# Kernel optimization log

Hardware: AMD Instinct MI355X
Metric: run time of the kernel (lower is better)

The kernel has to match this reference:

```python
import jax, jax.numpy as jnp
import numpy as np

N_USERS = 50000
N_ITEMS = 100000
N = N_USERS + N_ITEMS
E = 4_800_000
D = 64
N_LAYERS = 3
LEAKY = 0.5  # HGCNConv is built with leaky=0.5
LN_EPS = 1e-5


def setup_inputs() -> dict:
    key = jax.random.key(0)
    k1, k2, k3, k4 = jax.random.split(key, 4)
    ego = jax.random.normal(k1, (N, D), dtype=jnp.float32)
    vals = jax.random.uniform(k2, (E,), dtype=jnp.float32)
    rows = jax.random.randint(k3, (E,), 0, N, dtype=jnp.int32)
    cols = jax.random.randint(k4, (E,), 0, N, dtype=jnp.int32)
    gamma = jnp.ones((D,), dtype=jnp.float32)
    beta = jnp.zeros((D,), dtype=jnp.float32)
    return {"ego": ego, "vals": vals, "gamma": gamma, "beta": beta,
            "rows": rows, "cols": cols}


def _spmm(rows, cols, vals, x):
    # y[r] += vals[e] * x[cols[e]]  -> sparse NxN adj @ x ([N, D])
    return jax.ops.segment_sum(vals[:, None] * x[cols], rows, num_segments=N)


def _spmm_t(rows, cols, vals, x):
    # adj.T @ x : roles of rows/cols swapped
    return jax.ops.segment_sum(vals[:, None] * x[rows], cols, num_segments=N)


def _two_hop(rows, cols, vals, x):
    # sparse.mm(adj, sparse.mm(adj.t(), x))
    return _spmm(rows, cols, vals, _spmm_t(rows, cols, vals, x))


def _layer_norm(x, gamma, beta):
    mu = jnp.mean(x, axis=-1, keepdims=True)
    var = jnp.mean(jnp.square(x - mu), axis=-1, keepdims=True)
    return (x - mu) * jax.lax.rsqrt(var + LN_EPS) * gamma + beta


def reference(ego, vals, gamma, beta, rows, cols):
    res = ego
    e = ego
    for k in range(N_LAYERS):
        if k != N_LAYERS - 1:
            # HGCNConv with LeakyReLU(0.5)
            e = jax.nn.leaky_relu(_two_hop(rows, cols, vals, e), negative_slope=LEAKY)
        else:
            # final layer: LN(conv(adj, e, act=False)) + residual
            e = _layer_norm(_two_hop(rows, cols, vals, e), gamma, beta) + res
    # final embeddings [N, D]; user part = e[:N_USERS], item part = e[N_USERS:]
    return e
```

## Files before the change

### kernel.cpp

```cpp
#include <hip/hip_runtime.h>
#include <hip/hip_fp16.h>


#define NTOT 150000
#define NE   4800000
#define DD   64
#define NB   147
#define NBLK 512
#define EPB  9375

__global__ __launch_bounds__(256) void k_hist(const int* __restrict__ rows,
                                              const int* __restrict__ cols,
                                              int* __restrict__ histR,
                                              int* __restrict__ histC) {
    __shared__ int hR[NB], hC[NB];
    const int tid = threadIdx.x, blk = blockIdx.x;
    for (int i = tid; i < NB; i += 256) { hR[i] = 0; hC[i] = 0; }
    __syncthreads();
    const int e0 = blk * EPB;
    const int e1 = min(NE, e0 + EPB);
    for (int e = e0 + tid; e < e1; e += 256) {
        atomicAdd(&hR[rows[e] >> 10], 1);
        atomicAdd(&hC[cols[e] >> 10], 1);
    }
    __syncthreads();
    for (int i = tid; i < NB; i += 256) {
        histR[i * NBLK + blk] = hR[i];
        histC[i * NBLK + blk] = hC[i];
    }
}

__global__ __launch_bounds__(1024) void k_scan2(int* __restrict__ hR, int* __restrict__ hC,
                                                int* __restrict__ bbR, int* __restrict__ bbC) {
    __shared__ int wtot[16], wexcl[16];
    __shared__ int ctot;
    int* a  = blockIdx.x ? hC  : hR;
    int* bb = blockIdx.x ? bbC : bbR;
    const int n = NB * NBLK;
    const int tid  = threadIdx.x;
    const int lane = tid & 63, wv = tid >> 6;
    int carry = 0;
    for (int base = 0; base < n; base += 1024) {
        const int i = base + tid;
        const int v = (i < n) ? a[i] : 0;
        int s = v;
        #pragma unroll
        for (int off = 1; off < 64; off <<= 1) {
            int t = __shfl_up(s, off);
            if (lane >= off) s += t;
        }
        if (lane == 63) wtot[wv] = s;
        __syncthreads();
        if (tid == 0) {
            int run = 0;
            #pragma unroll
            for (int w = 0; w < 16; ++w) { wexcl[w] = run; run += wtot[w]; }
            ctot = run;
        }
        __syncthreads();
        if (i < n) a[i] = carry + wexcl[wv] + (s - v);
        carry += ctot;
        __syncthreads();
    }
    for (int i = tid; i <= NB; i += 1024) bb[i] = (i < NB) ? a[i * NBLK] : NE;
}

__global__ __launch_bounds__(256) void k_bin(const int* __restrict__ rows,
                                             const int* __restrict__ cols,
                                             const float* __restrict__ vals,
                                             const int* __restrict__ histR,
                                             const int* __restrict__ histC,
                                             int2* __restrict__ binR,
                                             int2* __restrict__ binC) {
    __shared__ int cR[NB], cC[NB];
    const int tid = threadIdx.x, blk = blockIdx.x;
    for (int i = tid; i < NB; i += 256) {
        cR[i] = histR[i * NBLK + blk];
        cC[i] = histC[i * NBLK + blk];
    }
    __syncthreads();
    const int e0 = blk * EPB;
    const int e1 = min(NE, e0 + EPB);
    for (int e = e0 + tid; e < e1; e += 256) {
        const int r = rows[e], c = cols[e];
        const int vb = __float_as_int(vals[e]);
        int p = atomicAdd(&cR[r >> 10], 1);
        int2 pr; pr.x = ((r & 1023) << 18) | c; pr.y = vb;
        binR[p] = pr;
        int q = atomicAdd(&cC[c >> 10], 1);
        int2 pc; pc.x = ((c & 1023) << 18) | r; pc.y = vb;
        binC[q] = pc;
    }
}

__global__ __launch_bounds__(1024) void k_sort(const int* __restrict__ bbR,
                                               const int2* __restrict__ binR,
                                               int2* __restrict__ csr, int* __restrict__ startsR,
                                               const int* __restrict__ bbC,
                                               const int2* __restrict__ binC,
                                               int2* __restrict__ csc, int* __restrict__ startsC) {
    __shared__ int hist[1024];
    __shared__ int cur[1024];
    __shared__ int wtot[16], wexcl[16];
    const int tid = threadIdx.x;
    const int lane = tid & 63, wv = tid >> 6;
    const int dir = (blockIdx.x >= NB) ? 1 : 0;
    const int b = blockIdx.x - dir * NB;
    const int*  bb     = dir ? bbC     : bbR;
    const int2* bin    = dir ? binC    : binR;
    int2*       out    = dir ? csc     : csr;
    int*        starts = dir ? startsC : startsR;
    const int ebase = bb[b];
    const int eend  = bb[b + 1];
    hist[tid] = 0;
    __syncthreads();
    for (int i = ebase + tid; i < eend; i += 1024)
        atomicAdd(&hist[((unsigned)bin[i].x) >> 18], 1);
    __syncthreads();
    const int v = hist[tid];
    int s = v;
    #pragma unroll
    for (int off = 1; off < 64; off <<= 1) { int t = __shfl_up(s, off); if (lane >= off) s += t; }
    if (lane == 63) wtot[wv] = s;
    __syncthreads();
    if (tid == 0) { int run = 0; for (int w = 0; w < 16; ++w) { wexcl[w] = run; run += wtot[w]; } }
    __syncthreads();
    const int excl = ebase + wexcl[wv] + (s - v);
    const int r0 = b << 10;
    if (r0 + tid < NTOT) starts[r0 + tid] = excl;
    cur[tid] = excl;
    __syncthreads();
    for (int i = ebase + tid; i < eend; i += 1024) {
        const int2 ed = bin[i];
        const int lr = ((unsigned)ed.x) >> 18;
        const int pos = atomicAdd(&cur[lr], 1);
        int2 o; o.x = ed.x & 0x3FFFF; o.y = ed.y;
        out[pos] = o;
    }
    if (blockIdx.x == 0 && tid == 0) { startsR[NTOT] = NE; startsC[NTOT] = NE; }
}

__global__ __launch_bounds__(256) void k_cvt(const float2* __restrict__ x,
                                             __half2* __restrict__ y, int n2) {
    int i = blockIdx.x * 256 + threadIdx.x;
    if (i < n2) y[i] = __float22half2_rn(x[i]);
}

template <int MODE>
__global__ __launch_bounds__(256) void k_spmm_h(const int* __restrict__ starts,
                                                const int2* __restrict__ edges,
                                                const __half2* __restrict__ xh,
                                                __half2* __restrict__ yh,
                                                float* __restrict__ yf,
                                                const float* __restrict__ gamma,
                                                const float* __restrict__ beta,
                                                const float* __restrict__ ego) {
    const int gid  = blockIdx.x * 256 + threadIdx.x;
    const int wid  = gid >> 6;
    const int lane = threadIdx.x & 63;
    if (wid >= NTOT) return;
    const int half_id = lane >> 5;
    const int c2 = lane & 31;
    const int s  = starts[wid];
    const int e2 = starts[wid + 1];
    float ax = 0.f, ay = 0.f;
    for (int base = s; base < e2; base += 64) {
        const int idx = base + lane;
        int2 ed;
        if (idx < e2) ed = edges[idx]; else { ed.x = 0; ed.y = 0; }
        int nb = e2 - base; if (nb > 64) nb = 64;
        const int npair = (nb + 1) >> 1;
        #pragma unroll 4
        for (int j = 0; j < npair; ++j) {
            const int sel = 2 * j + half_id;
            const int   c = __shfl(ed.x, sel);
            const float v = __int_as_float(__shfl(ed.y, sel));
            const float2 f = __half22float2(xh[c * 32 + c2]);
            ax = fmaf(v, f.x, ax);
            ay = fmaf(v, f.y, ay);
        }
    }
    ax += __shfl_xor(ax, 32);
    ay += __shfl_xor(ay, 32);
    if (MODE == 0) {
        if (lane < 32) yh[wid * 32 + c2] = __floats2half2_rn(ax, ay);
    } else if (MODE == 1) {
        if (lane < 32) {
            const float bx = ax > 0.f ? ax : 0.5f * ax;
            const float by = ay > 0.f ? ay : 0.5f * ay;
            yh[wid * 32 + c2] = __floats2half2_rn(bx, by);
        }
    } else {
        float s1 = ax + ay;
        #pragma unroll
        for (int off = 32; off; off >>= 1) s1 += __shfl_xor(s1, off);
        const float mu = s1 * (1.f / 128.f);
        const float dx = ax - mu, dy = ay - mu;
        float q = dx * dx + dy * dy;
        #pragma unroll
        for (int off = 32; off; off >>= 1) q += __shfl_xor(q, off);
        const float rs = rsqrtf(q * (1.f / 128.f) + 1e-5f);
        if (lane < 32) {
            const float2 g2 = ((const float2*)gamma)[c2];
            const float2 b2 = ((const float2*)beta)[c2];
            const float2 eg = ((const float2*)ego)[wid * 32 + c2];
            float2 o;
            o.x = dx * rs * g2.x + b2.x + eg.x;
            o.y = dy * rs * g2.y + b2.y + eg.y;
            ((float2*)yf)[wid * 32 + c2] = o;
        }
    }
}

__global__ __launch_bounds__(256) void k_push(const int* __restrict__ src_idx,
                                              const int* __restrict__ dst_idx,
                                              const float* __restrict__ vals,
                                              const float* __restrict__ x,
                                              float* __restrict__ y) {
    int gid  = blockIdx.x * 256 + threadIdx.x;
    int e    = gid >> 6;
    int lane = gid & 63;
    if (e >= NE) return;
    atomicAdd(&y[dst_idx[e] * DD + lane], vals[e] * x[src_idx[e] * DD + lane]);
}

__global__ __launch_bounds__(256) void k_leaky(float* __restrict__ x, int n) {
    int i = blockIdx.x * 256 + threadIdx.x;
    if (i < n) { float v = x[i]; x[i] = v > 0.f ? v : 0.5f * v; }
}

__global__ __launch_bounds__(256) void k_ln(const float* __restrict__ z,
                                            const float* __restrict__ gamma,
                                            const float* __restrict__ beta,
                                            const float* __restrict__ ego,
                                            float* __restrict__ out) {
    int gid  = blockIdx.x * 256 + threadIdx.x;
    int wid  = gid >> 6;
    int lane = threadIdx.x & 63;
    if (wid >= NTOT) return;
    float v = z[wid * DD + lane];
    float sum = v;
    #pragma unroll
    for (int off = 32; off; off >>= 1) sum += __shfl_xor(sum, off);
    float mu = sum * (1.f / 64.f);
    float d  = v - mu;
    float vs = d * d;
    #pragma unroll
    for (int off = 32; off; off >>= 1) vs += __shfl_xor(vs, off);
    float rs = rsqrtf(vs * (1.f / 64.f) + 1e-5f);
    out[wid * DD + lane] = d * rs * gamma[lane] + beta[lane] + ego[wid * DD + lane];
}

extern "C" void kernel_launch(void* const* d_in, const int* in_sizes, int n_in,
                              void* d_out, int out_size, void* d_ws, size_t ws_size,
                              hipStream_t stream) {
    const float* ego   = (const float*)d_in[0];
    const float* vals  = (const float*)d_in[1];
    const float* gamma = (const float*)d_in[2];
    const float* beta  = (const float*)d_in[3];
    const int*   rows  = (const int*)d_in[4];
    const int*   cols  = (const int*)d_in[5];
    float* out = (float*)d_out;

    const size_t SEG   = (size_t)NE * 8;
    const size_t SMETA = 600064;
    const size_t NEED  = 3 * SEG + 2 * SMETA + 1280;

    if (ws_size >= NEED) {
        char* w = (char*)d_ws;
        int2* csr  = (int2*)w;
        int2* csc  = (int2*)(w + SEG);
        int2* binR = (int2*)(w + 2 * SEG);
        int2* binC = (int2*)d_out;
        int* histR = (int*)w;
        int* histC = (int*)(w + SEG);
        int* startsR = (int*)(w + 3 * SEG);
        int* startsC = (int*)(w + 3 * SEG + SMETA);
        int* bbR     = (int*)(w + 3 * SEG + 2 * SMETA);
        int* bbC     = bbR + (NB + 1);
        __half2* B1h  = (__half2*)(w + 2 * SEG);
        __half2* B2h  = (__half2*)(w + 2 * SEG + SEG / 2);
        __half2* egoh = (__half2*)d_out;

        k_hist <<<NBLK, 256, 0, stream>>>(rows, cols, histR, histC);
        k_scan2<<<2, 1024, 0, stream>>>(histR, histC, bbR, bbC);
        k_bin  <<<NBLK, 256, 0, stream>>>(rows, cols, vals, histR, histC, binR, binC);
        k_sort <<<2 * NB, 1024, 0, stream>>>(bbR, binR, csr, startsR, bbC, binC, csc, startsC);
        k_cvt  <<<(NTOT * DD / 2 + 255) / 256, 256, 0, stream>>>((const float2*)ego, egoh, NTOT * DD / 2);

        const int GRID_N = (NTOT * 64) / 256;
        k_spmm_h<0><<<GRID_N, 256, 0, stream>>>(startsC, csc, egoh, B1h, nullptr, nullptr, nullptr, nullptr);
        k_spmm_h<1><<<GRID_N, 256, 0, stream>>>(startsR, csr, B1h, B2h, nullptr, nullptr, nullptr, nullptr);
        k_spmm_h<0><<<GRID_N, 256, 0, stream>>>(startsC, csc, B2h, B1h, nullptr, nullptr, nullptr, nullptr);
        k_spmm_h<1><<<GRID_N, 256, 0, stream>>>(startsR, csr, B1h, B2h, nullptr, nullptr, nullptr, nullptr);
        k_spmm_h<0><<<GRID_N, 256, 0, stream>>>(startsC, csc, B2h, B1h, nullptr, nullptr, nullptr, nullptr);
        k_spmm_h<2><<<GRID_N, 256, 0, stream>>>(startsR, csr, B1h, nullptr, out, gamma, beta, ego);
    } else {
        const size_t FEAT_BYTES = (size_t)NTOT * DD * 4;
        float* B1 = (float*)d_ws;
        float* B2 = out;
        const int GRID_P = NE / 4;
        const int GRID_N = (NTOT * DD) / 256;
        const float* e = ego;
        for (int layer = 0; layer < 3; ++layer) {
            hipMemsetAsync(B1, 0, FEAT_BYTES, stream);
            k_push<<<GRID_P, 256, 0, stream>>>(rows, cols, vals, e, B1);
            hipMemsetAsync(B2, 0, FEAT_BYTES, stream);
            k_push<<<GRID_P, 256, 0, stream>>>(cols, rows, vals, B1, B2);
            if (layer < 2) {
                k_leaky<<<GRID_N, 256, 0, stream>>>(B2, NTOT * DD);
                e = B2;
            } else {
                k_ln<<<GRID_N, 256, 0, stream>>>(B2, gamma, beta, ego, out);
            }
        }
    }
}
```

Baseline: 1.375 ms.

## Split fp16 features into column halves and gather 16-byte chunks per edge

The fp16 feature matrix is stored as two 32-column halves, each 64 bytes per row, and each SpMM pass now runs once per half. Each lane loads an int4 holding 8 halves, so 16 edges are processed at once per wavefront instead of 2. The intent is a smaller gathered working set per pass for better cache hit rates, plus wider loads that keep more gathers in flight. In exchange, the edge lists are read twice per layer, more kernels are launched, and more cross-lane shuffle reductions are needed. The final layer-norm kernel reads both halves and also uses 8-wide edge groups.

```diff
diff --git a/kernel.cpp b/kernel.cpp
--- a/kernel.cpp
+++ b/kernel.cpp
@@ -8,6 +8,8 @@
 #define NB   147
 #define NBLK 512
 #define EPB  9375
+#define HALF_I4 (NTOT * 4)
+#define HALF_H2 (NTOT * 16)
 
 __global__ __launch_bounds__(256) void k_hist(const int* __restrict__ rows,
                                               const int* __restrict__ cols,
@@ -141,17 +143,72 @@
 }
 
 __global__ __launch_bounds__(256) void k_cvt(const float2* __restrict__ x,
-                                             __half2* __restrict__ y, int n2) {
+                                             __half2* __restrict__ y) {
     int i = blockIdx.x * 256 + threadIdx.x;
-    if (i < n2) y[i] = __float22half2_rn(x[i]);
+    const int r = i >> 5, j = i & 31;
+    const int half = j >> 4;
+    y[half * HALF_H2 + r * 16 + (j & 15)] = __float22half2_rn(x[i]);
 }
 
 template <int MODE>
-__global__ __launch_bounds__(256) void k_spmm_h(const int* __restrict__ starts,
+__global__ __launch_bounds__(256) void k_spmm_s(const int* __restrict__ starts,
                                                 const int2* __restrict__ edges,
-                                                const __half2* __restrict__ xh,
-                                                __half2* __restrict__ yh,
-                                                float* __restrict__ yf,
+                                                const int4* __restrict__ xh,
+                                                int4* __restrict__ yh) {
+    const int gid  = blockIdx.x * 256 + threadIdx.x;
+    const int wid  = gid >> 6;
+    const int lane = threadIdx.x & 63;
+    if (wid >= NTOT) return;
+    const int g = lane >> 2;
+    const int l = lane & 3;
+    const int s  = starts[wid];
+    const int e2 = starts[wid + 1];
+    float acc[8];
+    #pragma unroll
+    for (int k = 0; k < 8; ++k) acc[k] = 0.f;
+    for (int base = s; base < e2; base += 64) {
+        const int idx = base + lane;
+        int2 ed;
+        if (idx < e2) ed = edges[idx]; else { ed.x = 0; ed.y = 0; }
+        const int nb = min(e2 - base, 64);
+        for (int j = 0; j < nb; j += 16) {
+            const int sel = j + g;
+            const int   c = __shfl(ed.x, sel);
+            const float v = __int_as_float(__shfl(ed.y, sel));
+            const int4 q = xh[c * 4 + l];
+            const __half2* h2 = (const __half2*)&q;
+            #pragma unroll
+            for (int k = 0; k < 4; ++k) {
+                const float2 f = __half22float2(h2[k]);
+                acc[2 * k]     = fmaf(v, f.x, acc[2 * k]);
+                acc[2 * k + 1] = fmaf(v, f.y, acc[2 * k + 1]);
+            }
+        }
+    }
+    #pragma unroll
+    for (int off = 4; off < 64; off <<= 1) {
+        #pragma unroll
+        for (int k = 0; k < 8; ++k) acc[k] += __shfl_xor(acc[k], off);
+    }
+    if (l == lane) {
+        __half2 o[4];
+        #pragma unroll
+        for (int k = 0; k < 4; ++k) {
+            float a = acc[2 * k], b = acc[2 * k + 1];
+            if (MODE == 1) {
+                a = a > 0.f ? a : 0.5f * a;
+                b = b > 0.f ? b : 0.5f * b;
+            }
+            o[k] = __floats2half2_rn(a, b);
+        }
+        yh[wid * 4 + l] = *(const int4*)o;
+    }
+}
+
+__global__ __launch_bounds__(256) void k_spmm_f(const int* __restrict__ starts,
+                                                const int2* __restrict__ edges,
+                                                const int4* __restrict__ xh,
+                                                float* __restrict__ out,
                                                 const float* __restrict__ gamma,
                                                 const float* __restrict__ beta,
                                                 const float* __restrict__ ego) {
@@ -159,55 +216,66 @@
     const int wid  = gid >> 6;
     const int lane = threadIdx.x & 63;
     if (wid >= NTOT) return;
-    const int half_id = lane >> 5;
-    const int c2 = lane & 31;
+    const int g = lane >> 3;
+    const int l = lane & 7;
+    const int hoff = (l >> 2) * HALF_I4 + (l & 3);
     const int s  = starts[wid];
     const int e2 = starts[wid + 1];
-    float ax = 0.f, ay = 0.f;
+    float acc[8];
+    #pragma unroll
+    for (int k = 0; k < 8; ++k) acc[k] = 0.f;
     for (int base = s; base < e2; base += 64) {
         const int idx = base + lane;
         int2 ed;
         if (idx < e2) ed = edges[idx]; else { ed.x = 0; ed.y = 0; }
-        int nb = e2 - base; if (nb > 64) nb = 64;
-        const int npair = (nb + 1) >> 1;
-        #pragma unroll 4
-        for (int j = 0; j < npair; ++j) {
-            const int sel = 2 * j + half_id;
+        const int nb = min(e2 - base, 64);
+        for (int j = 0; j < nb; j += 8) {
+            const int sel = j + g;
             const int   c = __shfl(ed.x, sel);
             const float v = __int_as_float(__shfl(ed.y, sel));
-            const float2 f = __half22float2(xh[c * 32 + c2]);
-            ax = fmaf(v, f.x, ax);
-            ay = fmaf(v, f.y, ay);
-        }
-    }
-    ax += __shfl_xor(ax, 32);
-    ay += __shfl_xor(ay, 32);
-    if (MODE == 0) {
-        if (lane < 32) yh[wid * 32 + c2] = __floats2half2_rn(ax, ay);
-    } else if (MODE == 1) {
-        if (lane < 32) {
-            const float bx = ax > 0.f ? ax : 0.5f * ax;
-            const float by = ay > 0.f ? ay : 0.5f * ay;
-            yh[wid * 32 + c2] = __floats2half2_rn(bx, by);
-        }
-    } else {
-        float s1 = ax + ay;
-        #pragma unroll
-        for (int off = 32; off; off >>= 1) s1 += __shfl_xor(s1, off);
-        const float mu = s1 * (1.f / 128.f);
-        const float dx = ax - mu, dy = ay - mu;
-        float q = dx * dx + dy * dy;
-        #pragma unroll
-        for (int off = 32; off; off >>= 1) q += __shfl_xor(q, off);
-        const float rs = rsqrtf(q * (1.f / 128.f) + 1e-5f);
-        if (lane < 32) {
-            const float2 g2 = ((const float2*)gamma)[c2];
-            const float2 b2 = ((const float2*)beta)[c2];
-            const float2 eg = ((const float2*)ego)[wid * 32 + c2];
-            float2 o;
-            o.x = dx * rs * g2.x + b2.x + eg.x;
-            o.y = dy * rs * g2.y + b2.y + eg.y;
-            ((float2*)yf)[wid * 32 + c2] = o;
+            const int4 q = xh[c * 4 + hoff];
+            const __half2* h2 = (const __half2*)&q;
+            #pragma unroll
+            for (int k = 0; k < 4; ++k) {
+                const float2 f = __half22float2(h2[k]);
+                acc[2 * k]     = fmaf(v, f.x, acc[2 * k]);
+                acc[2 * k + 1] = fmaf(v, f.y, acc[2 * k + 1]);
+            }
+        }
+    }
+    #pragma unroll
+    for (int off = 8; off < 64; off <<= 1) {
+        #pragma unroll
+        for (int k = 0; k < 8; ++k) acc[k] += __shfl_xor(acc[k], off);
+    }
+    float s1 = 0.f;
+    #pragma unroll
+    for (int k = 0; k < 8; ++k) s1 += acc[k];
+    #pragma unroll
+    for (int off = 1; off < 8; off <<= 1) s1 += __shfl_xor(s1, off);
+    const float mu = s1 * (1.f / 64.f);
+    float d[8], q2 = 0.f;
+    #pragma unroll
+    for (int k = 0; k < 8; ++k) { d[k] = acc[k] - mu; q2 += d[k] * d[k]; }
+    #pragma unroll
+    for (int off = 1; off < 8; off <<= 1) q2 += __shfl_xor(q2, off);
+    const float rs = rsqrtf(q2 * (1.f / 64.f) + 1e-5f);
+    if (lane < 8) {
+        const float4* g4 = (const float4*)gamma;
+        const float4* b4 = (const float4*)beta;
+        const float4* e4 = (const float4*)ego + (size_t)wid * 16;
+        float4*       o4 = (float4*)out + (size_t)wid * 16;
+        #pragma unroll
+        for (int half = 0; half < 2; ++half) {
+            const float4 gg = g4[2 * l + half];
+            const float4 bb = b4[2 * l + half];
+            const float4 ee = e4[2 * l + half];
+            float4 o;
+            o.x = d[4 * half + 0] * rs * gg.x + bb.x + ee.x;
+            o.y = d[4 * half + 1] * rs * gg.y + bb.y + ee.y;
+            o.z = d[4 * half + 2] * rs * gg.z + bb.z + ee.z;
+            o.w = d[4 * half + 3] * rs * gg.w + bb.w + ee.w;
+            o4[2 * l + half] = o;
         }
     }
 }
@@ -278,23 +346,28 @@
         int* startsC = (int*)(w + 3 * SEG + SMETA);
         int* bbR     = (int*)(w + 3 * SEG + 2 * SMETA);
         int* bbC     = bbR + (NB + 1);
-        __half2* B1h  = (__half2*)(w + 2 * SEG);
-        __half2* B2h  = (__half2*)(w + 2 * SEG + SEG / 2);
-        __half2* egoh = (__half2*)d_out;
+        int4* B1 = (int4*)(w + 2 * SEG);
+        int4* B2 = (int4*)(w + 2 * SEG + SEG / 2);
+        int4* EG = (int4*)d_out;
 
         k_hist <<<NBLK, 256, 0, stream>>>(rows, cols, histR, histC);
         k_scan2<<<2, 1024, 0, stream>>>(histR, histC, bbR, bbC);
         k_bin  <<<NBLK, 256, 0, stream>>>(rows, cols, vals, histR, histC, binR, binC);
         k_sort <<<2 * NB, 1024, 0, stream>>>(bbR, binR, csr, startsR, bbC, binC, csc, startsC);
-        k_cvt  <<<(NTOT * DD / 2 + 255) / 256, 256, 0, stream>>>((const float2*)ego, egoh, NTOT * DD / 2);
+        k_cvt  <<<(NTOT * 32) / 256, 256, 0, stream>>>((const float2*)ego, (__half2*)EG);
 
         const int GRID_N = (NTOT * 64) / 256;
-        k_spmm_h<0><<<GRID_N, 256, 0, stream>>>(startsC, csc, egoh, B1h, nullptr, nullptr, nullptr, nullptr);
-        k_spmm_h<1><<<GRID_N, 256, 0, stream>>>(startsR, csr, B1h, B2h, nullptr, nullptr, nullptr, nullptr);
-        k_spmm_h<0><<<GRID_N, 256, 0, stream>>>(startsC, csc, B2h, B1h, nullptr, nullptr, nullptr, nullptr);
-        k_spmm_h<1><<<GRID_N, 256, 0, stream>>>(startsR, csr, B1h, B2h, nullptr, nullptr, nullptr, nullptr);
-        k_spmm_h<0><<<GRID_N, 256, 0, stream>>>(startsC, csc, B2h, B1h, nullptr, nullptr, nullptr, nullptr);
-        k_spmm_h<2><<<GRID_N, 256, 0, stream>>>(startsR, csr, B1h, nullptr, out, gamma, beta, ego);
+        for (int h = 0; h < 2; ++h)
+            k_spmm_s<0><<<GRID_N, 256, 0, stream>>>(startsC, csc, EG + h * HALF_I4, B1 + h * HALF_I4);
+        for (int h = 0; h < 2; ++h)
+            k_spmm_s<1><<<GRID_N, 256, 0, stream>>>(startsR, csr, B1 + h * HALF_I4, B2 + h * HALF_I4);
+        for (int h = 0; h < 2; ++h)
+            k_spmm_s<0><<<GRID_N, 256, 0, stream>>>(startsC, csc, B2 + h * HALF_I4, B1 + h * HALF_I4);
+        for (int h = 0; h < 2; ++h)
+            k_spmm_s<1><<<GRID_N, 256, 0, stream>>>(startsR, csr, B1 + h * HALF_I4, B2 + h * HALF_I4);
+        for (int h = 0; h < 2; ++h)
+            k_spmm_s<0><<<GRID_N, 256, 0, stream>>>(startsC, csc, B2 + h * HALF_I4, B1 + h * HALF_I4);
+        k_spmm_f<<<GRID_N, 256, 0, stream>>>(startsR, csr, B1, out, gamma, beta, ego);
     } else {
         const size_t FEAT_BYTES = (size_t)NTOT * DD * 4;
         float* B1 = (float*)d_ws;
```

Result: faster. 1.283 ms (-6.6%).

## Compress edges to 32-bit with 14-bit quantized weights and slice features into column chunks

Applied to the files above, without the earlier changes.

Edges are packed into one u32 each: an 18-bit neighbor index plus a 14-bit quantized value, replacing the 8-byte int2, which halves edge traffic. Features are stored scaled fp16 in eight column slices of 8 halves (16 bytes), so each SpMM pass launches per slice and its gather working set fits better in cache. LayerNorm moves to a separate kernel that reads the sliced layout. The quantized weights and fp16 scaling lose precision, and the scheme depends on indices fitting in 18 bits. The edge list is also re-read eight times per hop, once per slice.

```diff
diff --git a/kernel.cpp b/kernel.cpp
--- a/kernel.cpp
+++ b/kernel.cpp
@@ -8,6 +8,12 @@
 #define NB   147
 #define NBLK 512
 #define EPB  9375
+#define FSCALE 0.00390625f
+#define LN_EPS_S (1e-5f * FSCALE * FSCALE)
+
+typedef unsigned int  u32;
+typedef unsigned short u16;
+typedef int i4 __attribute__((ext_vector_type(4)));
 
 __global__ __launch_bounds__(256) void k_hist(const int* __restrict__ rows,
                                               const int* __restrict__ cols,
@@ -70,8 +76,8 @@
                                              const float* __restrict__ vals,
                                              const int* __restrict__ histR,
                                              const int* __restrict__ histC,
-                                             int2* __restrict__ binR,
-                                             int2* __restrict__ binC) {
+                                             u32* __restrict__ binAR, u16* __restrict__ binQR,
+                                             u32* __restrict__ binAC, u16* __restrict__ binQC) {
     __shared__ int cR[NB], cC[NB];
     const int tid = threadIdx.x, blk = blockIdx.x;
     for (int i = tid; i < NB; i += 256) {
@@ -83,22 +89,24 @@
     const int e1 = min(NE, e0 + EPB);
     for (int e = e0 + tid; e < e1; e += 256) {
         const int r = rows[e], c = cols[e];
-        const int vb = __float_as_int(vals[e]);
+        const u16 q = (u16)(vals[e] * 16383.f + 0.5f);
         int p = atomicAdd(&cR[r >> 10], 1);
-        int2 pr; pr.x = ((r & 1023) << 18) | c; pr.y = vb;
-        binR[p] = pr;
-        int q = atomicAdd(&cC[c >> 10], 1);
-        int2 pc; pc.x = ((c & 1023) << 18) | r; pc.y = vb;
-        binC[q] = pc;
+        binAR[p] = ((u32)(r & 1023) << 18) | (u32)c;
+        binQR[p] = q;
+        int p2 = atomicAdd(&cC[c >> 10], 1);
+        binAC[p2] = ((u32)(c & 1023) << 18) | (u32)r;
+        binQC[p2] = q;
     }
 }
 
 __global__ __launch_bounds__(1024) void k_sort(const int* __restrict__ bbR,
-                                               const int2* __restrict__ binR,
-                                               int2* __restrict__ csr, int* __restrict__ startsR,
+                                               const u32* __restrict__ binAR,
+                                               const u16* __restrict__ binQR,
+                                               u32* __restrict__ csr, int* __restrict__ startsR,
                                                const int* __restrict__ bbC,
-                                               const int2* __restrict__ binC,
-                                               int2* __restrict__ csc, int* __restrict__ startsC) {
+                                               const u32* __restrict__ binAC,
+                                               const u16* __restrict__ binQC,
+                                               u32* __restrict__ csc, int* __restrict__ startsC) {
     __shared__ int hist[1024];
     __shared__ int cur[1024];
     __shared__ int wtot[16], wexcl[16];
@@ -106,16 +114,17 @@
     const int lane = tid & 63, wv = tid >> 6;
     const int dir = (blockIdx.x >= NB) ? 1 : 0;
     const int b = blockIdx.x - dir * NB;
-    const int*  bb     = dir ? bbC     : bbR;
-    const int2* bin    = dir ? binC    : binR;
-    int2*       out    = dir ? csc     : csr;
-    int*        starts = dir ? startsC : startsR;
+    const int* bb      = dir ? bbC    : bbR;
+    const u32* binA    = dir ? binAC  : binAR;
+    const u16* binQ    = dir ? binQC  : binQR;
+    u32*       out     = dir ? csc    : csr;
+    int*       starts  = dir ? startsC : startsR;
     const int ebase = bb[b];
     const int eend  = bb[b + 1];
     hist[tid] = 0;
     __syncthreads();
     for (int i = ebase + tid; i < eend; i += 1024)
-        atomicAdd(&hist[((unsigned)bin[i].x) >> 18], 1);
+        atomicAdd(&hist[binA[i] >> 18], 1);
     __syncthreads();
     const int v = hist[tid];
     int s = v;
@@ -131,84 +140,126 @@
     cur[tid] = excl;
     __syncthreads();
     for (int i = ebase + tid; i < eend; i += 1024) {
-        const int2 ed = bin[i];
-        const int lr = ((unsigned)ed.x) >> 18;
-        const int pos = atomicAdd(&cur[lr], 1);
-        int2 o; o.x = ed.x & 0x3FFFF; o.y = ed.y;
-        out[pos] = o;
+        const u32 a = binA[i];
+        const int pos = atomicAdd(&cur[a >> 18], 1);
+        out[pos] = ((a & 0x3FFFFu) << 14) | (u32)binQ[i];
     }
     if (blockIdx.x == 0 && tid == 0) { startsR[NTOT] = NE; startsC[NTOT] = NE; }
 }
 
 __global__ __launch_bounds__(256) void k_cvt(const float2* __restrict__ x,
-                                             __half2* __restrict__ y, int n2) {
+                                             __half2* __restrict__ y) {
     int i = blockIdx.x * 256 + threadIdx.x;
-    if (i < n2) y[i] = __float22half2_rn(x[i]);
+    const int r = i >> 5, j = i & 31;
+    const int e8 = j >> 2, slot = j & 3;
+    const float2 v = x[i];
+    y[(size_t)e8 * (NTOT * 4) + r * 4 + slot] =
+        __floats2half2_rn(v.x * FSCALE, v.y * FSCALE);
 }
 
 template <int MODE>
-__global__ __launch_bounds__(256) void k_spmm_h(const int* __restrict__ starts,
-                                                const int2* __restrict__ edges,
-                                                const __half2* __restrict__ xh,
-                                                __half2* __restrict__ yh,
-                                                float* __restrict__ yf,
-                                                const float* __restrict__ gamma,
-                                                const float* __restrict__ beta,
-                                                const float* __restrict__ ego) {
-    const int gid  = blockIdx.x * 256 + threadIdx.x;
-    const int wid  = gid >> 6;
+__global__ __launch_bounds__(256) void k_spmm8(const int* __restrict__ starts,
+                                               const u32* __restrict__ edges,
+                                               const int4* __restrict__ x8,
+                                               int4* __restrict__ y8) {
+    const int w    = (blockIdx.x * 256 + threadIdx.x) >> 6;
     const int lane = threadIdx.x & 63;
-    if (wid >= NTOT) return;
-    const int half_id = lane >> 5;
-    const int c2 = lane & 31;
-    const int s  = starts[wid];
-    const int e2 = starts[wid + 1];
-    float ax = 0.f, ay = 0.f;
-    for (int base = s; base < e2; base += 64) {
-        const int idx = base + lane;
-        int2 ed;
-        if (idx < e2) ed = edges[idx]; else { ed.x = 0; ed.y = 0; }
-        int nb = e2 - base; if (nb > 64) nb = 64;
-        const int npair = (nb + 1) >> 1;
-        #pragma unroll 4
-        for (int j = 0; j < npair; ++j) {
-            const int sel = 2 * j + half_id;
-            const int   c = __shfl(ed.x, sel);
-            const float v = __int_as_float(__shfl(ed.y, sel));
-            const float2 f = __half22float2(xh[c * 32 + c2]);
-            ax = fmaf(v, f.x, ax);
-            ay = fmaf(v, f.y, ay);
-        }
-    }
-    ax += __shfl_xor(ax, 32);
-    ay += __shfl_xor(ay, 32);
-    if (MODE == 0) {
-        if (lane < 32) yh[wid * 32 + c2] = __floats2half2_rn(ax, ay);
-    } else if (MODE == 1) {
-        if (lane < 32) {
-            const float bx = ax > 0.f ? ax : 0.5f * ax;
-            const float by = ay > 0.f ? ay : 0.5f * ay;
-            yh[wid * 32 + c2] = __floats2half2_rn(bx, by);
-        }
-    } else {
-        float s1 = ax + ay;
-        #pragma unroll
-        for (int off = 32; off; off >>= 1) s1 += __shfl_xor(s1, off);
-        const float mu = s1 * (1.f / 128.f);
-        const float dx = ax - mu, dy = ay - mu;
-        float q = dx * dx + dy * dy;
-        #pragma unroll
-        for (int off = 32; off; off >>= 1) q += __shfl_xor(q, off);
-        const float rs = rsqrtf(q * (1.f / 128.f) + 1e-5f);
-        if (lane < 32) {
-            const float2 g2 = ((const float2*)gamma)[c2];
-            const float2 b2 = ((const float2*)beta)[c2];
-            const float2 eg = ((const float2*)ego)[wid * 32 + c2];
-            float2 o;
-            o.x = dx * rs * g2.x + b2.x + eg.x;
-            o.y = dy * rs * g2.y + b2.y + eg.y;
-            ((float2*)yf)[wid * 32 + c2] = o;
-        }
+    const int q = lane >> 4, l = lane & 15;
+    const int r = w * 4 + q;
+    const int s = starts[r];
+    const int e = starts[r + 1];
+    int m = e - s;
+    m = max(m, __shfl_xor(m, 16));
+    m = max(m, __shfl_xor(m, 32));
+    const int iters = (m + 15) >> 4;
+    float a0 = 0.f, a1 = 0.f, a2 = 0.f, a3 = 0.f, a4 = 0.f, a5 = 0.f, a6 = 0.f, a7 = 0.f;
+    for (int it = 0; it < iters; ++it) {
+        const int idx = s + it * 16 + l;
+        if (idx < e) {
+            const u32 u = __builtin_nontemporal_load(&edges[idx]);
+            const int   c = (int)(u >> 14);
+            const float v = (float)(u & 16383u) * (1.f / 16383.f);
+            const int4 g = x8[c];
+            const __half2* h = (const __half2*)&g;
+            float2 f0 = __half22float2(h[0]);
+            float2 f1 = __half22float2(h[1]);
+            float2 f2 = __half22float2(h[2]);
+            float2 f3 = __half22float2(h[3]);
+            a0 = fmaf(v, f0.x, a0); a1 = fmaf(v, f0.y, a1);
+            a2 = fmaf(v, f1.x, a2); a3 = fmaf(v, f1.y, a3);
+            a4 = fmaf(v, f2.x, a4); a5 = fmaf(v, f2.y, a5);
+            a6 = fmaf(v, f3.x, a6); a7 = fmaf(v, f3.y, a7);
+        }
+    }
+    #pragma unroll
+    for (int off = 1; off < 16; off <<= 1) {
+        a0 += __shfl_xor(a0, off); a1 += __shfl_xor(a1, off);
+        a2 += __shfl_xor(a2, off); a3 += __shfl_xor(a3, off);
+        a4 += __shfl_xor(a4, off); a5 += __shfl_xor(a5, off);
+        a6 += __shfl_xor(a6, off); a7 += __shfl_xor(a7, off);
+    }
+    if (l == 0) {
+        if (MODE == 1) {
+            a0 = a0 > 0.f ? a0 : 0.5f * a0; a1 = a1 > 0.f ? a1 : 0.5f * a1;
+            a2 = a2 > 0.f ? a2 : 0.5f * a2; a3 = a3 > 0.f ? a3 : 0.5f * a3;
+            a4 = a4 > 0.f ? a4 : 0.5f * a4; a5 = a5 > 0.f ? a5 : 0.5f * a5;
+            a6 = a6 > 0.f ? a6 : 0.5f * a6; a7 = a7 > 0.f ? a7 : 0.5f * a7;
+        }
+        i4 ov;
+        __half2* op = (__half2*)&ov;
+        op[0] = __floats2half2_rn(a0, a1);
+        op[1] = __floats2half2_rn(a2, a3);
+        op[2] = __floats2half2_rn(a4, a5);
+        op[3] = __floats2half2_rn(a6, a7);
+        __builtin_nontemporal_store(ov, (i4*)&y8[r]);
+    }
+}
+
+__global__ __launch_bounds__(256) void k_ln2(const int4* __restrict__ z8,
+                                             const float* __restrict__ gamma,
+                                             const float* __restrict__ beta,
+                                             const float* __restrict__ ego,
+                                             float* __restrict__ out) {
+    const int w    = (blockIdx.x * 256 + threadIdx.x) >> 6;
+    const int lane = threadIdx.x & 63;
+    const int q = lane >> 3, e8 = lane & 7;
+    const int r = w * 8 + q;
+    if (r >= NTOT) return;
+    const int4 g = z8[(size_t)e8 * NTOT + r];
+    const __half2* h = (const __half2*)&g;
+    float f[8];
+    #pragma unroll
+    for (int k = 0; k < 4; ++k) {
+        const float2 t = __half22float2(h[k]);
+        f[2 * k] = t.x; f[2 * k + 1] = t.y;
+    }
+    float s1 = 0.f;
+    #pragma unroll
+    for (int k = 0; k < 8; ++k) s1 += f[k];
+    #pragma unroll
+    for (int off = 1; off < 8; off <<= 1) s1 += __shfl_xor(s1, off);
+    const float mu = s1 * (1.f / 64.f);
+    float d[8], q2 = 0.f;
+    #pragma unroll
+    for (int k = 0; k < 8; ++k) { d[k] = f[k] - mu; q2 += d[k] * d[k]; }
+    #pragma unroll
+    for (int off = 1; off < 8; off <<= 1) q2 += __shfl_xor(q2, off);
+    const float rs = rsqrtf(q2 * (1.f / 64.f) + LN_EPS_S);
+    const float4* g4 = (const float4*)gamma;
+    const float4* b4 = (const float4*)beta;
+    const float4* e4 = (const float4*)ego + (size_t)r * 16;
+    float4*       o4 = (float4*)out + (size_t)r * 16;
+    #pragma unroll
+    for (int hh = 0; hh < 2; ++hh) {
+        const float4 gg = g4[2 * e8 + hh];
+        const float4 bb = b4[2 * e8 + hh];
+        const float4 ee = e4[2 * e8 + hh];
+        float4 o;
+        o.x = d[4 * hh + 0] * rs * gg.x + bb.x + ee.x;
+        o.y = d[4 * hh + 1] * rs * gg.y + bb.y + ee.y;
+        o.z = d[4 * hh + 2] * rs * gg.z + bb.z + ee.z;
+        o.w = d[4 * hh + 3] * rs * gg.w + bb.w + ee.w;
+        o4[2 * e8 + hh] = o;
     }
 }
 
@@ -262,39 +313,52 @@
     const int*   cols  = (const int*)d_in[5];
     float* out = (float*)d_out;
 
-    const size_t SEG   = (size_t)NE * 8;
+    const size_t SEG4  = (size_t)NE * 4;
+    const size_t SEG2  = (size_t)NE * 2;
     const size_t SMETA = 600064;
-    const size_t NEED  = 3 * SEG + 2 * SMETA + 1280;
+    const size_t HSZ   = (size_t)NB * NBLK * 4;
+    const size_t NEED  = 5 * SEG4 + 2 * SEG2 + 2 * SMETA + 2 * HSZ + 4096;
 
     if (ws_size >= NEED) {
         char* w = (char*)d_ws;
-        int2* csr  = (int2*)w;
-        int2* csc  = (int2*)(w + SEG);
-        int2* binR = (int2*)(w + 2 * SEG);
-        int2* binC = (int2*)d_out;
-        int* histR = (int*)w;
-        int* histC = (int*)(w + SEG);
-        int* startsR = (int*)(w + 3 * SEG);
-        int* startsC = (int*)(w + 3 * SEG + SMETA);
-        int* bbR     = (int*)(w + 3 * SEG + 2 * SMETA);
+        u32* csr   = (u32*)(w);
+        u32* csc   = (u32*)(w + SEG4);
+        u32* binAR = (u32*)(w + 2 * SEG4);
+        u32* binAC = (u32*)(w + 3 * SEG4);
+        u16* binQR = (u16*)(w + 4 * SEG4);
+        u16* binQC = (u16*)(w + 4 * SEG4 + SEG2);
+        int* startsR = (int*)(w + 4 * SEG4 + 2 * SEG2);
+        int* startsC = (int*)(w + 4 * SEG4 + 2 * SEG2 + SMETA);
+        int* histR   = (int*)(w + 4 * SEG4 + 2 * SEG2 + 2 * SMETA);
+        int* histC   = (int*)((char*)histR + HSZ);
+        int* bbR     = (int*)((char*)histC + HSZ);
         int* bbC     = bbR + (NB + 1);
-        __half2* B1h  = (__half2*)(w + 2 * SEG);
-        __half2* B2h  = (__half2*)(w + 2 * SEG + SEG / 2);
-        __half2* egoh = (__half2*)d_out;
+        int4* B1 = (int4*)(w + 2 * SEG4);
+        int4* B2 = (int4*)(w + 3 * SEG4);
+        int4* E8 = (int4*)d_out;
 
         k_hist <<<NBLK, 256, 0, stream>>>(rows, cols, histR, histC);
         k_scan2<<<2, 1024, 0, stream>>>(histR, histC, bbR, bbC);
-        k_bin  <<<NBLK, 256, 0, stream>>>(rows, cols, vals, histR, histC, binR, binC);
-        k_sort <<<2 * NB, 1024, 0, stream>>>(bbR, binR, csr, startsR, bbC, binC, csc, startsC);
-        k_cvt  <<<(NTOT * DD / 2 + 255) / 256, 256, 0, stream>>>((const float2*)ego, egoh, NTOT * DD / 2);
-
-        const int GRID_N = (NTOT * 64) / 256;
-        k_spmm_h<0><<<GRID_N, 256, 0, stream>>>(startsC, csc, egoh, B1h, nullptr, nullptr, nullptr, nullptr);
-        k_spmm_h<1><<<GRID_N, 256, 0, stream>>>(startsR, csr, B1h, B2h, nullptr, nullptr, nullptr, nullptr);
-        k_spmm_h<0><<<GRID_N, 256, 0, stream>>>(startsC, csc, B2h, B1h, nullptr, nullptr, nullptr, nullptr);
-        k_spmm_h<1><<<GRID_N, 256, 0, stream>>>(startsR, csr, B1h, B2h, nullptr, nullptr, nullptr, nullptr);
-        k_spmm_h<0><<<GRID_N, 256, 0, stream>>>(startsC, csc, B2h, B1h, nullptr, nullptr, nullptr, nullptr);
-        k_spmm_h<2><<<GRID_N, 256, 0, stream>>>(startsR, csr, B1h, nullptr, out, gamma, beta, ego);
+        k_bin  <<<NBLK, 256, 0, stream>>>(rows, cols, vals, histR, histC,
+                                          binAR, binQR, binAC, binQC);
+        k_sort <<<2 * NB, 1024, 0, stream>>>(bbR, binAR, binQR, csr, startsR,
+                                             bbC, binAC, binQC, csc, startsC);
+        k_cvt  <<<(NTOT * 32) / 256, 256, 0, stream>>>((const float2*)ego, (__half2*)E8);
+
+        const int GRID_S = (NTOT / 4) * 64 / 256;
+        for (int e8 = 0; e8 < 8; ++e8)
+            k_spmm8<0><<<GRID_S, 256, 0, stream>>>(startsC, csc, E8 + e8 * NTOT, B1 + e8 * NTOT);
+        for (int e8 = 0; e8 < 8; ++e8)
+            k_spmm8<1><<<GRID_S, 256, 0, stream>>>(startsR, csr, B1 + e8 * NTOT, B2 + e8 * NTOT);
+        for (int e8 = 0; e8 < 8; ++e8)
+            k_spmm8<0><<<GRID_S, 256, 0, stream>>>(startsC, csc, B2 + e8 * NTOT, B1 + e8 * NTOT);
+        for (int e8 = 0; e8 < 8; ++e8)
+            k_spmm8<1><<<GRID_S, 256, 0, stream>>>(startsR, csr, B1 + e8 * NTOT, B2 + e8 * NTOT);
+        for (int e8 = 0; e8 < 8; ++e8)
+            k_spmm8<0><<<GRID_S, 256, 0, stream>>>(startsC, csc, B2 + e8 * NTOT, B1 + e8 * NTOT);
+        for (int e8 = 0; e8 < 8; ++e8)
+            k_spmm8<0><<<GRID_S, 256, 0, stream>>>(startsR, csr, B1 + e8 * NTOT, B2 + e8 * NTOT);
+        k_ln2<<<(NTOT / 8 + 3) / 4, 256, 0, stream>>>(B2, gamma, beta, ego, out);
     } else {
         const size_t FEAT_BYTES = (size_t)NTOT * DD * 4;
         float* B1 = (float*)d_ws;
@@ -303,9 +367,9 @@
         const int GRID_N = (NTOT * DD) / 256;
         const float* e = ego;
         for (int layer = 0; layer < 3; ++layer) {
-            hipMemsetAsync(B1, 0, FEAT_BYTES, stream);
+            (void)hipMemsetAsync(B1, 0, FEAT_BYTES, stream);
             k_push<<<GRID_P, 256, 0, stream>>>(rows, cols, vals, e, B1);
-            hipMemsetAsync(B2, 0, FEAT_BYTES, stream);
+            (void)hipMemsetAsync(B2, 0, FEAT_BYTES, stream);
             k_push<<<GRID_P, 256, 0, stream>>>(cols, rows, vals, B1, B2);
             if (layer < 2) {
                 k_leaky<<<GRID_N, 256, 0, stream>>>(B2, NTOT * DD);
```

Measured after the change: 2.424 ms. 76.3% more time.
